# Optimization experiments

Hardware: AMD Instinct MI355X
Metric: run time of the kernel (lower is better)

Reference implementation:

```python
import jax, jax.numpy as jnp
import numpy as np
import math

B, T, D = 2, 2048, 1024
H, HD = 16, 64
MAX_LEN = 2048


def _build_rope_sin_cos(max_seq, head_dim):
    inv_freq = 1.0 / 10000 ** (jnp.arange(0, head_dim, 2) / head_dim)
    positions = jnp.arange(max_seq)
    sinusoid_inp = jnp.einsum('i,j->ij', positions.astype(jnp.float32), inv_freq.astype(jnp.float32))
    sin = jnp.repeat(jnp.sin(sinusoid_inp), 2, axis=-1)
    cos = jnp.repeat(jnp.cos(sinusoid_inp), 2, axis=-1)
    return sin, cos


def _rotate_half(x):
    x1 = x[..., ::2]
    x2 = x[..., 1::2]
    return jnp.stack((-x2, x1), axis=-1).reshape(x.shape)


def setup_inputs() -> dict:
    key = jax.random.key(0)
    ks = jax.random.split(key, 6)
    x = jax.random.normal(ks[0], (B, T, D), dtype=jnp.float32)
    # causal boolean mask (B, T, T)
    mask = jnp.broadcast_to(jnp.tril(jnp.ones((T, T), dtype=bool)), (B, T, T))
    s = 1.0 / math.sqrt(D)
    wq = jax.random.normal(ks[1], (D, H, HD), dtype=jnp.float32) * s
    wk = jax.random.normal(ks[2], (D, H, HD), dtype=jnp.float32) * s
    wv = jax.random.normal(ks[3], (D, H, HD), dtype=jnp.float32) * s
    wo = jax.random.normal(ks[4], (H * HD, D), dtype=jnp.float32) * (1.0 / math.sqrt(H * HD))
    return {"x": x, "mask": mask, "wq": wq, "wk": wk, "wv": wv, "wo": wo}


def reference(x, mask, wq, wk, wv, wo):
    Bx, Tx, Dx = x.shape
    # q/k/v projections: DenseGeneral D -> (H, HD)
    q = jnp.einsum('btd,dhe->bthe', x, wq)
    k = jnp.einsum('btd,dhe->bthe', x, wk)
    v = jnp.einsum('btd,dhe->bthe', x, wv)
    sin, cos = _build_rope_sin_cos(MAX_LEN, HD)
    sin_t = sin[:Tx][None, :, None, :]
    cos_t = cos[:Tx][None, :, None, :]
    q = q * cos_t + _rotate_half(q) * sin_t
    k = k * cos_t + _rotate_half(k) * sin_t
    q = jnp.transpose(q, (0, 2, 1, 3))  # (B,H,T,HD)
    k = jnp.transpose(k, (0, 2, 1, 3))
    v = jnp.transpose(v, (0, 2, 1, 3))
    scale = 1.0 / math.sqrt(HD)
    logits = jnp.einsum('bhqd,bhkd->bhqk', q, k) * scale
    mask_f = mask[:, None, :, :].astype(jnp.float32)
    logits = logits + (1.0 - mask_f) * -1e10
    w = jax.nn.softmax(logits, axis=-1)
    attn_out = jnp.einsum('bhqk,bhkd->bhqd', w, v)
    attn_out = jnp.transpose(attn_out, (0, 2, 1, 3)).reshape(Bx, Tx, -1)
    return attn_out @ wo
```

## Files before the change

### kernel.cpp

```cpp
#include <hip/hip_runtime.h>
#include <cstdint>
#include <cstddef>

typedef __bf16 bf16x8 __attribute__((ext_vector_type(8)));
typedef __bf16 bf16x2 __attribute__((ext_vector_type(2)));
typedef float f32x4 __attribute__((ext_vector_type(4)));
typedef float f32x16 __attribute__((ext_vector_type(16)));
typedef unsigned int u32x4 __attribute__((ext_vector_type(4)));
#define UNROLL _Pragma("unroll")

__device__ __forceinline__ unsigned short f2bf(float f) {
  unsigned int x = __builtin_bit_cast(unsigned int, f);
  x += 0x7fffu + ((x >> 16) & 1u);
  return (unsigned short)(x >> 16);
}
__device__ __forceinline__ float bf2f(unsigned short u) {
  return __builtin_bit_cast(float, (unsigned int)u << 16);
}
__device__ __forceinline__ unsigned int cvtpk(float a, float b) {
  bf16x2 t; t[0] = (__bf16)a; t[1] = (__bf16)b;
  return __builtin_bit_cast(unsigned int, t);
}
__device__ __forceinline__ void async16(const void* g, void* l) {
  __builtin_amdgcn_global_load_lds((void __attribute__((address_space(1)))*)g,
                                   (void __attribute__((address_space(3)))*)l,
                                   16, 0, 0);
}

__global__ void prep_x(const float* __restrict__ x, unsigned short* __restrict__ xb) {
  int i = blockIdx.x * 256 + threadIdx.x;
  const float4* p = (const float4*)(x + (size_t)i * 8);
  float4 a = p[0], b = p[1];
  ushort4 o0 = {f2bf(a.x), f2bf(a.y), f2bf(a.z), f2bf(a.w)};
  ushort4 o1 = {f2bf(b.x), f2bf(b.y), f2bf(b.z), f2bf(b.w)};
  ushort4* q = (ushort4*)(xb + (size_t)i * 8);
  q[0] = o0; q[1] = o1;
}

__global__ void prep_w(const float* __restrict__ wq, const float* __restrict__ wk,
                       const float* __restrict__ wv, const float* __restrict__ wo,
                       unsigned short* __restrict__ out) {
  __shared__ float tile[32][33];
  const float* src = blockIdx.z == 0 ? wq : blockIdx.z == 1 ? wk : blockIdx.z == 2 ? wv : wo;
  unsigned short* dst = out + (size_t)blockIdx.z * 1048576;
  int kb = blockIdx.x * 32, nb = blockIdx.y * 32;
  int c = threadIdx.x & 31, r4 = (threadIdx.x >> 5) * 4;
UNROLL
  for (int i = 0; i < 4; ++i)
    tile[r4 + i][c] = src[(size_t)(kb + r4 + i) * 1024 + nb + c];
  __syncthreads();
UNROLL
  for (int i = 0; i < 4; ++i)
    dst[(size_t)(nb + r4 + i) * 1024 + kb + c] = f2bf(tile[c][r4 + i]);
}

__global__ void prep_rope(float2* __restrict__ tab) {
  int idx = blockIdx.x * 256 + threadIdx.x;
  int t = idx >> 5, i = idx & 31;
  float inv = exp2f(-(float)i * (13.287712379549449f / 32.0f));
  float ang = (float)t * inv;
  tab[idx] = make_float2(cosf(ang), sinf(ang));
}

__global__ __launch_bounds__(256, 3) void gemmqkv(
    const unsigned short* __restrict__ A, const unsigned short* __restrict__ Bt,
    unsigned short* __restrict__ qout, unsigned short* __restrict__ kout,
    unsigned short* __restrict__ vtout, const float2* __restrict__ rope) {
  __shared__ __align__(16) unsigned short As[128 * 64];
  __shared__ __align__(16) unsigned short Bs[128 * 64];
  const int tid = threadIdx.x;
  const int lane = tid & 63, wid = tid >> 6;
  const int wr = wid >> 1, wc = wid & 1;
  const int g = lane >> 4, r16 = lane & 15;
  const int m0 = blockIdx.y * 128, n0 = blockIdx.x * 128;

  f32x4 acc[4][4];
UNROLL
  for (int i = 0; i < 4; ++i)
UNROLL
    for (int j = 0; j < 4; ++j) acc[i][j] = (f32x4){0.f, 0.f, 0.f, 0.f};

  const int ce = (((tid & 7) ^ ((tid >> 3) & 7)) << 3);
  const unsigned short* gA = A + (size_t)(m0 + (tid >> 3)) * 1024 + ce;
  const unsigned short* gB = Bt + (size_t)(n0 + (tid >> 3)) * 1024 + ce;
  char* lA = (char*)As + tid * 16;
  char* lB = (char*)Bs + tid * 16;

  const int swz = (r16 & 7) << 4;

  for (int u = 0; u < 16; ++u) {
    const int k0 = u * 64;
UNROLL
    for (int s = 0; s < 4; ++s) {
      async16(gA + (size_t)s * 32 * 1024 + k0, lA + s * 4096);
      async16(gB + (size_t)s * 32 * 1024 + k0, lB + s * 4096);
    }
    __syncthreads();
UNROLL
    for (int kk = 0; kk < 2; ++kk) {
      bf16x8 af[4], bfr[4];
UNROLL
      for (int mi = 0; mi < 4; ++mi)
        af[mi] = *(const bf16x8*)((const char*)As +
                  (wr * 64 + mi * 16 + r16) * 128 + ((kk * 64 + g * 16) ^ swz));
UNROLL
      for (int ni = 0; ni < 4; ++ni)
        bfr[ni] = *(const bf16x8*)((const char*)Bs +
                  (wc * 64 + ni * 16 + r16) * 128 + ((kk * 64 + g * 16) ^ swz));
UNROLL
      for (int mi = 0; mi < 4; ++mi)
UNROLL
        for (int ni = 0; ni < 4; ++ni)
          acc[mi][ni] = __builtin_amdgcn_mfma_f32_16x16x32_bf16(af[mi], bfr[ni],
                                                                acc[mi][ni], 0, 0, 0);
    }
    __syncthreads();
  }

  const int which = n0 >> 10;
  const int b = (m0 >= 2048) ? 1 : 0;
  const float QSCL = 0.18033688011112042f;
UNROLL
  for (int mi = 0; mi < 4; ++mi) {
    const int rowb = m0 + wr * 64 + mi * 16 + g * 4;
    const int trow = rowb & 2047;
UNROLL
    for (int ni = 0; ni < 4; ++ni) {
      const int n = n0 + wc * 64 + ni * 16 + r16;
      const int h = (n >> 6) & 15, e = n & 63;
      f32x4 v = acc[mi][ni];
      if (which < 2) {
        const int fi = e >> 1;
        const bool ev = (e & 1) == 0;
UNROLL
        for (int j = 0; j < 4; ++j) {
          float2 cs = rope[(trow + j) * 32 + fi];
          float p = __shfl_xor(v[j], 1);
          v[j] = ev ? (v[j] * cs.x - p * cs.y) : (v[j] * cs.x + p * cs.y);
        }
        if (which == 0) { v[0] *= QSCL; v[1] *= QSCL; v[2] *= QSCL; v[3] *= QSCL; }
      }
      if (which == 2) {
        size_t base = (((size_t)b * 16 + h) * 64 + e) * 2048 + trow;
        ushort4 pkv = {f2bf(v[0]), f2bf(v[1]), f2bf(v[2]), f2bf(v[3])};
        *(ushort4*)(vtout + base) = pkv;
      } else {
        unsigned short* dst = (which == 0) ? qout : kout;
        size_t base = (((size_t)b * 16 + h) * 2048 + trow) * 64 + e;
UNROLL
        for (int j = 0; j < 4; ++j) dst[base + (size_t)j * 64] = f2bf(v[j]);
      }
    }
  }
}

__global__ __launch_bounds__(256, 4) void gemm_o(
    const unsigned short* __restrict__ A, const unsigned short* __restrict__ Bt,
    float* __restrict__ out) {
  __shared__ __align__(16) unsigned short As[2][64 * 64];
  __shared__ __align__(16) unsigned short Bs[2][64 * 64];
  const int tid = threadIdx.x;
  const int lane = tid & 63, wid = tid >> 6;
  const int wm = wid >> 1, wn = wid & 1;
  const int g = lane >> 4, r16 = lane & 15;
  const int m0 = blockIdx.y * 64, n0 = blockIdx.x * 64;

  f32x4 acc[2][2];
UNROLL
  for (int i = 0; i < 2; ++i)
UNROLL
    for (int j = 0; j < 2; ++j) acc[i][j] = (f32x4){0.f, 0.f, 0.f, 0.f};

  const int ce = (((tid & 7) ^ ((tid >> 3) & 7)) << 3);
  const unsigned short* gA = A + (size_t)(m0 + (tid >> 3)) * 1024 + ce;
  const unsigned short* gB = Bt + (size_t)(n0 + (tid >> 3)) * 1024 + ce;
  const int dst0 = tid * 16;
  const int swz = (r16 & 7) << 4;

#define OSTG(bb, koff) { \
    async16(gA + (koff),             (char*)As[bb] + dst0); \
    async16(gA + 32 * 1024 + (koff), (char*)As[bb] + dst0 + 4096); \
    async16(gB + (koff),             (char*)Bs[bb] + dst0); \
    async16(gB + 32 * 1024 + (koff), (char*)Bs[bb] + dst0 + 4096); }

  OSTG(0, 0)
  for (int u = 0; u < 16; ++u) {
    const int bsel = u & 1;
    if (u + 1 < 16) { OSTG(bsel ^ 1, (u + 1) * 64) }
    __builtin_amdgcn_sched_barrier(0);
    if (u + 1 < 16) { asm volatile("s_waitcnt vmcnt(4)" ::: "memory"); }
    else            { asm volatile("s_waitcnt vmcnt(0)" ::: "memory"); }
    __builtin_amdgcn_s_barrier();
    __builtin_amdgcn_sched_barrier(0);
UNROLL
    for (int kk = 0; kk < 2; ++kk) {
      bf16x8 af[2], bfr[2];
UNROLL
      for (int mi = 0; mi < 2; ++mi)
        af[mi] = *(const bf16x8*)((const char*)As[bsel] +
                  (wm * 32 + mi * 16 + r16) * 128 + ((kk * 64 + g * 16) ^ swz));
UNROLL
      for (int ni = 0; ni < 2; ++ni)
        bfr[ni] = *(const bf16x8*)((const char*)Bs[bsel] +
                  (wn * 32 + ni * 16 + r16) * 128 + ((kk * 64 + g * 16) ^ swz));
UNROLL
      for (int mi = 0; mi < 2; ++mi)
UNROLL
        for (int ni = 0; ni < 2; ++ni)
          acc[mi][ni] = __builtin_amdgcn_mfma_f32_16x16x32_bf16(af[mi], bfr[ni],
                                                                acc[mi][ni], 0, 0, 0);
    }
    __builtin_amdgcn_sched_barrier(0);
    __builtin_amdgcn_s_barrier();
  }
#undef OSTG

UNROLL
  for (int mi = 0; mi < 2; ++mi) {
    const int rowb = m0 + wm * 32 + mi * 16 + g * 4;
UNROLL
    for (int ni = 0; ni < 2; ++ni) {
      const int n = n0 + wn * 32 + ni * 16 + r16;
UNROLL
      for (int j = 0; j < 4; ++j)
        out[(size_t)(rowb + j) * 1024 + n] = acc[mi][ni][j];
    }
  }
}

__device__ const signed char c_qt[32]   = {15,15,10,10,15,14,14,14,13, 9, 9, 4,13,13,12,12, 8, 8,12,11,11,11, 7, 7, 3, 6, 6, 5, 5, 2, 1, 0};
__device__ const signed char c_t0[32]   = { 0,11, 0,11,22, 0,10,20, 0, 0,10, 0,10,19, 0, 9, 0, 9,18, 0, 8,16, 0, 8, 0, 0, 7, 0, 6, 0, 0, 0};
__device__ const signed char c_len[32]  = {11,11,11,11,10,10,10,10,10,10,10,10, 9, 9, 9, 9, 9, 9, 8, 8, 8, 8, 8, 8, 8, 7, 7, 6, 6, 6, 4, 2};
__device__ const signed char c_slot[32] = {24,25,10,11,26,21,22,23,18, 8, 9,-1,19,20,15,16, 6, 7,17,12,13,14, 4, 5,-1, 2, 3, 0, 1,-1,-1,-1};

__global__ __launch_bounds__(256, 4) void attn4(
    const unsigned short* __restrict__ qb, const unsigned short* __restrict__ kb,
    const unsigned short* __restrict__ vtb, unsigned short* __restrict__ attnb,
    unsigned short* __restrict__ po, float* __restrict__ ml) {
  __shared__ __align__(16) char smem[2][16384];
  const int tid = threadIdx.x;
  const int lane = tid & 63, w = tid >> 6;
  const int l31 = lane & 31, h = lane >> 5;
  const int bh = blockIdx.x;
  const int item = blockIdx.y;
  const int qt = c_qt[item];
  const int t0 = c_t0[item];
  const int t1 = t0 + c_len[item];
  const int slot = c_slot[item];
  const int q0w = qt * 128 + w * 32;
  const int qg = q0w + l31;
  const size_t kvbase = (size_t)bh * (2048 * 64);
  const float NFM = -11.0f;

  bf16x8 qf[4];
  const unsigned short* qp = qb + kvbase + (size_t)qg * 64 + h * 8;
UNROLL
  for (int kk = 0; kk < 4; ++kk) qf[kk] = *(const bf16x8*)(qp + kk * 16);

  const int lr = lane >> 3;
  const int cb2 = ((lane & 7) ^ lr) << 3;
  const bool isK = (w < 2);
  const int c0 = isK ? w * 4 : (w - 2) * 4;
  const unsigned short* srcp[4];
  int dstoff[4];
  const size_t step = isK ? 4096 : 64;
UNROLL
  for (int s = 0; s < 4; ++s) {
    int r = (c0 + s) * 8 + lr;
    srcp[s] = isK ? (kb + kvbase + (size_t)r * 64 + cb2)
                  : (vtb + kvbase + (size_t)r * 2048 + cb2);
    dstoff[s] = (w * 4 + s) * 1024 + lane * 16;
  }

  f32x16 o0, o1;
UNROLL
  for (int r = 0; r < 16; ++r) { o0[r] = 0.f; o1[r] = 0.f; }
  float l_run = 0.f;

UNROLL
  for (int s = 0; s < 4; ++s) async16(srcp[s] + (size_t)t0 * step, &smem[0][0] + dstoff[s]);

  const int swz = (l31 & 7) << 4;
  for (int t = t0; t < t1; ++t) {
    const int kt0 = t << 6;
    if (t + 1 < t1) {
      char* db = &smem[(t + 1 - t0) & 1][0];
UNROLL
      for (int s = 0; s < 4; ++s)
        async16(srcp[s] + (size_t)(t + 1) * step, db + dstoff[s]);
      __builtin_amdgcn_sched_barrier(0);
      asm volatile("s_waitcnt vmcnt(4)" ::: "memory");
    } else {
      __builtin_amdgcn_sched_barrier(0);
      asm volatile("s_waitcnt vmcnt(0)" ::: "memory");
    }
    __builtin_amdgcn_s_barrier();
    __builtin_amdgcn_sched_barrier(0);
    if (kt0 <= q0w + 31) {
      const char* cbuf = &smem[(t - t0) & 1][0];
      f32x16 sa, sb;
UNROLL
      for (int r = 0; r < 16; ++r) { sa[r] = NFM; sb[r] = NFM; }
      __builtin_amdgcn_s_setprio(1);
UNROLL
      for (int kk = 0; kk < 4; ++kk) {
        bf16x8 kf = *(const bf16x8*)(cbuf + l31 * 128 + ((kk * 32 + h * 16) ^ swz));
        sa = __builtin_amdgcn_mfma_f32_32x32x16_bf16(kf, qf[kk], sa, 0, 0, 0);
      }
UNROLL
      for (int kk = 0; kk < 4; ++kk) {
        bf16x8 kf = *(const bf16x8*)(cbuf + (32 + l31) * 128 + ((kk * 32 + h * 16) ^ swz));
        sb = __builtin_amdgcn_mfma_f32_32x32x16_bf16(kf, qf[kk], sb, 0, 0, 0);
      }
      __builtin_amdgcn_s_setprio(0);
      if (kt0 + 63 > q0w) {
UNROLL
        for (int r = 0; r < 16; ++r) {
          int koff = (r & 3) + 8 * (r >> 2) + 4 * h;
          if (kt0 + koff > qg) sa[r] = -3e38f;
          if (kt0 + 32 + koff > qg) sb[r] = -3e38f;
        }
      }
UNROLL
      for (int r = 0; r < 16; ++r) {
        sa[r] = exp2f(sa[r]);
        sb[r] = exp2f(sb[r]);
      }
      float ts[16];
UNROLL
      for (int i = 0; i < 16; ++i) ts[i] = sa[i] + sb[i];
UNROLL
      for (int i = 0; i < 8; ++i) ts[i] += ts[i + 8];
UNROLL
      for (int i = 0; i < 4; ++i) ts[i] += ts[i + 4];
      ts[0] += ts[2]; ts[1] += ts[3];
      float ps = ts[0] + ts[1];
      ps += __shfl_xor(ps, 32);
      l_run += ps;
      unsigned int lo[8], hi[8];
UNROLL
      for (int b8 = 0; b8 < 4; ++b8) {
        lo[b8]     = cvtpk(sa[4 * b8], sa[4 * b8 + 1]);
        hi[b8]     = cvtpk(sa[4 * b8 + 2], sa[4 * b8 + 3]);
        lo[4 + b8] = cvtpk(sb[4 * b8], sb[4 * b8 + 1]);
        hi[4 + b8] = cvtpk(sb[4 * b8 + 2], sb[4 * b8 + 3]);
      }
      bf16x8 pa[4];
UNROLL
      for (int j = 0; j < 4; ++j) {
        const int bb = (j >> 1) * 4 + (j & 1) * 2;
        unsigned int a0 = lo[bb], b0 = lo[bb + 1];
        unsigned int a1 = hi[bb], b1 = hi[bb + 1];
        asm volatile("v_permlane32_swap_b32 %0, %1" : "+v"(a0), "+v"(b0));
        asm volatile("v_permlane32_swap_b32 %0, %1" : "+v"(a1), "+v"(b1));
        u32x4 f;
        f[0] = a0; f[1] = a1; f[2] = b0; f[3] = b1;
        pa[j] = __builtin_bit_cast(bf16x8, f);
      }
      __builtin_amdgcn_s_setprio(1);
UNROLL
      for (int j = 0; j < 4; ++j) {
        bf16x8 v0 = *(const bf16x8*)(cbuf + 8192 + l31 * 128 + ((j * 32 + h * 16) ^ swz));
        bf16x8 v1 = *(const bf16x8*)(cbuf + 8192 + (32 + l31) * 128 + ((j * 32 + h * 16) ^ swz));
        o0 = __builtin_amdgcn_mfma_f32_32x32x16_bf16(pa[j], v0, o0, 0, 0, 0);
        o1 = __builtin_amdgcn_mfma_f32_32x32x16_bf16(pa[j], v1, o1, 0, 0, 0);
      }
      __builtin_amdgcn_s_setprio(0);
    }
    __builtin_amdgcn_sched_barrier(0);
    __builtin_amdgcn_s_barrier();
  }

  float* lsh = (float*)&smem[0][0] + w * 32;
  if (h == 0) lsh[l31] = 1.0f / l_run;
  __syncthreads();
  f32x4 inv[4];
UNROLL
  for (int rg = 0; rg < 4; ++rg) inv[rg] = *(const f32x4*)&lsh[8 * rg + 4 * h];
  if (slot < 0) {
    const int b = bh >> 4, hh = bh & 15;
UNROLL
    for (int r = 0; r < 16; ++r) {
      const int qg2 = q0w + (r & 3) + 8 * (r >> 2) + 4 * h;
      const size_t base = (((size_t)b * 2048 + qg2) * 16 + hh) * 64 + l31;
      const float iv = inv[r >> 2][r & 3];
      attnb[base]      = f2bf(o0[r] * iv);
      attnb[base + 32] = f2bf(o1[r] * iv);
    }
  } else {
    const int p = bh * 27 + slot;
    if (h == 0) ml[p * 128 + w * 32 + l31] = l_run;
    unsigned short* pb = po + (size_t)p * 8192;
UNROLL
    for (int r = 0; r < 16; ++r) {
      const int rl = w * 32 + (r & 3) + 8 * (r >> 2) + 4 * h;
      const float iv = inv[r >> 2][r & 3];
      pb[rl * 64 + l31]      = f2bf(o0[r] * iv);
      pb[rl * 64 + l31 + 32] = f2bf(o1[r] * iv);
    }
  }
}

__global__ void attn_combine(const unsigned short* __restrict__ po,
                             const float* __restrict__ ml,
                             unsigned short* __restrict__ attnb) {
  const int idx = blockIdx.x * 256 + threadIdx.x;
  const int cg = idx & 3;
  const int row = (idx >> 2) & 127;
  const int t2 = idx >> 9;
  const int qi = t2 % 11;
  const int bh = t2 / 11;
  const int qt = qi + 5;
  const int cnt = (qt < 11) ? 2 : 3;
  const int base = (qt < 11) ? (qt - 5) * 2 : 12 + (qt - 11) * 3;
  const int slotg = bh * 27 + base;
  float acc[16];
UNROLL
  for (int i = 0; i < 16; ++i) acc[i] = 0.f;
  float wsum = 0.f;
  for (int i = 0; i < cnt; ++i) {
    const float l = ml[(slotg + i) * 128 + row];
    wsum += l;
    const ushort4* p = (const ushort4*)(po + (size_t)(slotg + i) * 8192 + row * 64 + cg * 16);
UNROLL
    for (int v = 0; v < 4; ++v) {
      ushort4 u = p[v];
      acc[v * 4 + 0] += l * bf2f(u.x);
      acc[v * 4 + 1] += l * bf2f(u.y);
      acc[v * 4 + 2] += l * bf2f(u.z);
      acc[v * 4 + 3] += l * bf2f(u.w);
    }
  }
  const float inv = 1.0f / wsum;
  const int b = bh >> 4, hh = bh & 15;
  const int q = qt * 128 + row;
  ushort4* out = (ushort4*)(attnb + (((size_t)b * 2048 + q) * 16 + hh) * 64 + cg * 16);
UNROLL
  for (int v = 0; v < 4; ++v) {
    ushort4 o;
    o.x = f2bf(acc[v * 4 + 0] * inv);
    o.y = f2bf(acc[v * 4 + 1] * inv);
    o.z = f2bf(acc[v * 4 + 2] * inv);
    o.w = f2bf(acc[v * 4 + 3] * inv);
    out[v] = o;
  }
}

extern "C" void kernel_launch(void* const* d_in, const int* in_sizes, int n_in,
                              void* d_out, int out_size, void* d_ws, size_t ws_size,
                              hipStream_t stream) {
  (void)in_sizes; (void)n_in; (void)out_size; (void)ws_size;
  const float* x = (const float*)d_in[0];
  const float* wq = (const float*)d_in[2];
  const float* wk = (const float*)d_in[3];
  const float* wv = (const float*)d_in[4];
  const float* wo = (const float*)d_in[5];

  unsigned short* xb = (unsigned short*)d_ws;
  unsigned short* wT = xb + 4 * 1024 * 1024;
  float2* rope = (float2*)(wT + 4 * 1024 * 1024);
  unsigned short* qb = (unsigned short*)(rope + 65536);
  unsigned short* kbuf = qb + 4 * 1024 * 1024;
  unsigned short* vtb = kbuf + 4 * 1024 * 1024;
  unsigned short* attnb = vtb + 4 * 1024 * 1024;

  unsigned short* po = xb;
  float* mlb = (float*)rope;

  prep_x<<<dim3(2048), dim3(256), 0, stream>>>(x, xb);
  prep_w<<<dim3(32, 32, 4), dim3(256), 0, stream>>>(wq, wk, wv, wo, wT);
  prep_rope<<<dim3(256), dim3(256), 0, stream>>>(rope);
  gemmqkv<<<dim3(24, 32), dim3(256), 0, stream>>>(xb, wT, qb, kbuf, vtb, rope);
  attn4<<<dim3(32, 32), dim3(256), 0, stream>>>(qb, kbuf, vtb, attnb, po, mlb);
  attn_combine<<<dim3(704), dim3(256), 0, stream>>>(po, mlb, attnb);
  gemm_o<<<dim3(16, 64), dim3(256), 0, stream>>>(attnb, wT + 3 * 1024 * 1024,
                                                 (float*)d_out);
}
```

Measured before the change: 111.5 us.

## Double-buffer QKV GEMM K-loop and compute softmax row sums via MFMA

The QKV projection GEMM now stages 32-wide K slices into two LDS buffers and prefetches the next slice while computing the current one, using explicit vmcnt waits instead of a load-then-sync loop. In attention, the per-row softmax denominator is accumulated by an extra MFMA against a ones vector, replacing the VALU reduction tree and cross-lane shuffle, and the shared-memory broadcast of inverse sums is dropped. The fixed -11 logit offset is removed, so scores start from zero. This adds one MFMA per PV step and shifts the GEMM to smaller K chunks with more barriers. It also relies on the bf16 rounded probabilities for the row sums, which may slightly change numerics.

```diff
diff --git a/kernel.cpp b/kernel.cpp
--- a/kernel.cpp
+++ b/kernel.cpp
@@ -66,8 +66,8 @@
     const unsigned short* __restrict__ A, const unsigned short* __restrict__ Bt,
     unsigned short* __restrict__ qout, unsigned short* __restrict__ kout,
     unsigned short* __restrict__ vtout, const float2* __restrict__ rope) {
-  __shared__ __align__(16) unsigned short As[128 * 64];
-  __shared__ __align__(16) unsigned short Bs[128 * 64];
+  __shared__ __align__(16) unsigned short As[2][128 * 32];
+  __shared__ __align__(16) unsigned short Bs[2][128 * 32];
   const int tid = threadIdx.x;
   const int lane = tid & 63, wid = tid >> 6;
   const int wr = wid >> 1, wc = wid & 1;
@@ -80,42 +80,46 @@
 UNROLL
     for (int j = 0; j < 4; ++j) acc[i][j] = (f32x4){0.f, 0.f, 0.f, 0.f};
 
-  const int ce = (((tid & 7) ^ ((tid >> 3) & 7)) << 3);
-  const unsigned short* gA = A + (size_t)(m0 + (tid >> 3)) * 1024 + ce;
-  const unsigned short* gB = Bt + (size_t)(n0 + (tid >> 3)) * 1024 + ce;
-  char* lA = (char*)As + tid * 16;
-  char* lB = (char*)Bs + tid * 16;
-
-  const int swz = (r16 & 7) << 4;
-
-  for (int u = 0; u < 16; ++u) {
-    const int k0 = u * 64;
-UNROLL
-    for (int s = 0; s < 4; ++s) {
-      async16(gA + (size_t)s * 32 * 1024 + k0, lA + s * 4096);
-      async16(gB + (size_t)s * 32 * 1024 + k0, lB + s * 4096);
-    }
-    __syncthreads();
-UNROLL
-    for (int kk = 0; kk < 2; ++kk) {
-      bf16x8 af[4], bfr[4];
-UNROLL
-      for (int mi = 0; mi < 4; ++mi)
-        af[mi] = *(const bf16x8*)((const char*)As +
-                  (wr * 64 + mi * 16 + r16) * 128 + ((kk * 64 + g * 16) ^ swz));
+  const int ce = (((tid & 3) ^ ((tid >> 2) & 3)) << 3);
+  const unsigned short* gA = A + (size_t)(m0 + (tid >> 2)) * 1024 + ce;
+  const unsigned short* gB = Bt + (size_t)(n0 + (tid >> 2)) * 1024 + ce;
+  const int dst0 = tid * 16;
+  const int swz = (r16 & 3) << 4;
+
+#define QSTG(bb, koff) { \
+    async16(gA + (koff),             (char*)As[bb] + dst0); \
+    async16(gA + 64 * 1024 + (koff), (char*)As[bb] + dst0 + 4096); \
+    async16(gB + (koff),             (char*)Bs[bb] + dst0); \
+    async16(gB + 64 * 1024 + (koff), (char*)Bs[bb] + dst0 + 4096); }
+
+  QSTG(0, 0)
+  for (int u = 0; u < 32; ++u) {
+    const int bsel = u & 1;
+    if (u + 1 < 32) { QSTG(bsel ^ 1, (u + 1) * 32) }
+    __builtin_amdgcn_sched_barrier(0);
+    if (u + 1 < 32) { asm volatile("s_waitcnt vmcnt(4)" ::: "memory"); }
+    else            { asm volatile("s_waitcnt vmcnt(0)" ::: "memory"); }
+    __builtin_amdgcn_s_barrier();
+    __builtin_amdgcn_sched_barrier(0);
+    bf16x8 af[4], bfr[4];
+UNROLL
+    for (int mi = 0; mi < 4; ++mi)
+      af[mi] = *(const bf16x8*)((const char*)As[bsel] +
+                (wr * 64 + mi * 16 + r16) * 64 + ((g * 16) ^ swz));
+UNROLL
+    for (int ni = 0; ni < 4; ++ni)
+      bfr[ni] = *(const bf16x8*)((const char*)Bs[bsel] +
+                (wc * 64 + ni * 16 + r16) * 64 + ((g * 16) ^ swz));
+UNROLL
+    for (int mi = 0; mi < 4; ++mi)
 UNROLL
       for (int ni = 0; ni < 4; ++ni)
-        bfr[ni] = *(const bf16x8*)((const char*)Bs +
-                  (wc * 64 + ni * 16 + r16) * 128 + ((kk * 64 + g * 16) ^ swz));
-UNROLL
-      for (int mi = 0; mi < 4; ++mi)
-UNROLL
-        for (int ni = 0; ni < 4; ++ni)
-          acc[mi][ni] = __builtin_amdgcn_mfma_f32_16x16x32_bf16(af[mi], bfr[ni],
-                                                                acc[mi][ni], 0, 0, 0);
-    }
-    __syncthreads();
-  }
+        acc[mi][ni] = __builtin_amdgcn_mfma_f32_16x16x32_bf16(af[mi], bfr[ni],
+                                                              acc[mi][ni], 0, 0, 0);
+    __builtin_amdgcn_sched_barrier(0);
+    __builtin_amdgcn_s_barrier();
+  }
+#undef QSTG
 
   const int which = n0 >> 10;
   const int b = (m0 >= 2048) ? 1 : 0;
@@ -250,12 +254,14 @@
   const int q0w = qt * 128 + w * 32;
   const int qg = q0w + l31;
   const size_t kvbase = (size_t)bh * (2048 * 64);
-  const float NFM = -11.0f;
 
   bf16x8 qf[4];
   const unsigned short* qp = qb + kvbase + (size_t)qg * 64 + h * 8;
 UNROLL
   for (int kk = 0; kk < 4; ++kk) qf[kk] = *(const bf16x8*)(qp + kk * 16);
+
+  u32x4 of; of[0] = of[1] = of[2] = of[3] = 0x3F803F80u;
+  const bf16x8 onesf = __builtin_bit_cast(bf16x8, of);
 
   const int lr = lane >> 3;
   const int cb2 = ((lane & 7) ^ lr) << 3;
@@ -272,10 +278,9 @@
     dstoff[s] = (w * 4 + s) * 1024 + lane * 16;
   }
 
-  f32x16 o0, o1;
-UNROLL
-  for (int r = 0; r < 16; ++r) { o0[r] = 0.f; o1[r] = 0.f; }
-  float l_run = 0.f;
+  f32x16 o0, o1, lacc;
+UNROLL
+  for (int r = 0; r < 16; ++r) { o0[r] = 0.f; o1[r] = 0.f; lacc[r] = 0.f; }
 
 UNROLL
   for (int s = 0; s < 4; ++s) async16(srcp[s] + (size_t)t0 * step, &smem[0][0] + dstoff[s]);
@@ -300,7 +305,7 @@
       const char* cbuf = &smem[(t - t0) & 1][0];
       f32x16 sa, sb;
 UNROLL
-      for (int r = 0; r < 16; ++r) { sa[r] = NFM; sb[r] = NFM; }
+      for (int r = 0; r < 16; ++r) { sa[r] = 0.f; sb[r] = 0.f; }
       __builtin_amdgcn_s_setprio(1);
 UNROLL
       for (int kk = 0; kk < 4; ++kk) {
@@ -326,17 +331,6 @@
         sa[r] = exp2f(sa[r]);
         sb[r] = exp2f(sb[r]);
       }
-      float ts[16];
-UNROLL
-      for (int i = 0; i < 16; ++i) ts[i] = sa[i] + sb[i];
-UNROLL
-      for (int i = 0; i < 8; ++i) ts[i] += ts[i + 8];
-UNROLL
-      for (int i = 0; i < 4; ++i) ts[i] += ts[i + 4];
-      ts[0] += ts[2]; ts[1] += ts[3];
-      float ps = ts[0] + ts[1];
-      ps += __shfl_xor(ps, 32);
-      l_run += ps;
       unsigned int lo[8], hi[8];
 UNROLL
       for (int b8 = 0; b8 < 4; ++b8) {
@@ -364,6 +358,7 @@
         bf16x8 v1 = *(const bf16x8*)(cbuf + 8192 + (32 + l31) * 128 + ((j * 32 + h * 16) ^ swz));
         o0 = __builtin_amdgcn_mfma_f32_32x32x16_bf16(pa[j], v0, o0, 0, 0, 0);
         o1 = __builtin_amdgcn_mfma_f32_32x32x16_bf16(pa[j], v1, o1, 0, 0, 0);
+        lacc = __builtin_amdgcn_mfma_f32_32x32x16_bf16(pa[j], onesf, lacc, 0, 0, 0);
       }
       __builtin_amdgcn_s_setprio(0);
     }
@@ -371,30 +366,28 @@
     __builtin_amdgcn_s_barrier();
   }
 
-  float* lsh = (float*)&smem[0][0] + w * 32;
-  if (h == 0) lsh[l31] = 1.0f / l_run;
-  __syncthreads();
-  f32x4 inv[4];
-UNROLL
-  for (int rg = 0; rg < 4; ++rg) inv[rg] = *(const f32x4*)&lsh[8 * rg + 4 * h];
   if (slot < 0) {
     const int b = bh >> 4, hh = bh & 15;
 UNROLL
     for (int r = 0; r < 16; ++r) {
       const int qg2 = q0w + (r & 3) + 8 * (r >> 2) + 4 * h;
       const size_t base = (((size_t)b * 2048 + qg2) * 16 + hh) * 64 + l31;
-      const float iv = inv[r >> 2][r & 3];
+      const float iv = 1.0f / lacc[r];
       attnb[base]      = f2bf(o0[r] * iv);
       attnb[base + 32] = f2bf(o1[r] * iv);
     }
   } else {
     const int p = bh * 27 + slot;
-    if (h == 0) ml[p * 128 + w * 32 + l31] = l_run;
+    if (l31 == 0) {
+UNROLL
+      for (int r = 0; r < 16; ++r)
+        ml[p * 128 + w * 32 + (r & 3) + 8 * (r >> 2) + 4 * h] = lacc[r];
+    }
     unsigned short* pb = po + (size_t)p * 8192;
 UNROLL
     for (int r = 0; r < 16; ++r) {
       const int rl = w * 32 + (r & 3) + 8 * (r >> 2) + 4 * h;
-      const float iv = inv[r >> 2][r & 3];
+      const float iv = 1.0f / lacc[r];
       pb[rl * 64 + l31]      = f2bf(o0[r] * iv);
       pb[rl * 64 + l31 + 32] = f2bf(o1[r] * iv);
     }
```

After: 115.4 us. 1.04x slower.
